# Kernel tuning notes

Measured on AMD Instinct MI355X. Metric: run time of the kernel, lower is better.

The kernel has to match this reference:

```python
import jax, jax.numpy as jnp
import numpy as np

N_NODES = 100000
C = 128
E = 800000
V = 50000
NEG_SLOPE = 0.2


def gat_conv(x, edges, W, att_src, att_dst, bias, num_nodes):
    """Single-head PyG-style GATConv with self-loops added (PyG default).

    edges: [2, E] with row 0 = source j, row 1 = destination i.
    """
    loops = jnp.arange(num_nodes, dtype=edges.dtype)
    src = jnp.concatenate([edges[0], loops])  # [E+N]
    dst = jnp.concatenate([edges[1], loops])

    h = x @ W.T                               # [N, C] linear transform
    a_s = h @ att_src                         # [N] per-node src score
    a_d = h @ att_dst                         # [N] per-node dst score

    e = jax.nn.leaky_relu(a_s[src] + a_d[dst], NEG_SLOPE)  # [E+N]
    # scatter-softmax over edges grouped by destination node
    m = jax.ops.segment_max(e, dst, num_segments=num_nodes)
    ex = jnp.exp(e - m[dst])
    denom = jax.ops.segment_sum(ex, dst, num_segments=num_nodes)
    alpha = ex / (denom[dst] + 1e-16)         # [E+N]

    out = jax.ops.segment_sum(alpha[:, None] * h[src], dst, num_segments=num_nodes)
    return out + bias


def setup_inputs() -> dict:
    key = jax.random.key(0)
    ks = jax.random.split(key, 12)
    s = 1.0 / np.sqrt(C)
    return {
        "embedding": jax.random.normal(ks[0], (N_NODES, C), jnp.float32),
        "W1": jax.random.normal(ks[1], (C, C), jnp.float32) * s,
        "att_src1": jax.random.normal(ks[2], (C,), jnp.float32) * s,
        "att_dst1": jax.random.normal(ks[3], (C,), jnp.float32) * s,
        "b1": jax.random.normal(ks[4], (C,), jnp.float32) * s,
        "W2": jax.random.normal(ks[5], (C, C), jnp.float32) * s,
        "att_src2": jax.random.normal(ks[6], (C,), jnp.float32) * s,
        "att_dst2": jax.random.normal(ks[7], (C,), jnp.float32) * s,
        "b2": jax.random.normal(ks[8], (C,), jnp.float32) * s,
        "edges1": jax.random.randint(ks[9], (2, E), 0, N_NODES, jnp.int64 if jax.config.jax_enable_x64 else jnp.int32),
        "edges2": jax.random.randint(ks[10], (2, E), 0, N_NODES, jnp.int64 if jax.config.jax_enable_x64 else jnp.int32),
        "idx_mapping": jax.random.randint(ks[11], (V,), 0, N_NODES, jnp.int64 if jax.config.jax_enable_x64 else jnp.int32),
    }


def reference(embedding, W1, att_src1, att_dst1, b1, W2, att_src2, att_dst2, b2,
              edges1, edges2, idx_mapping):
    h = gat_conv(embedding, edges1, W1, att_src1, att_dst1, b1, N_NODES)
    h = gat_conv(h, edges2, W2, att_src2, att_dst2, b2, N_NODES)
    return h[idx_mapping]
```

## Files before the change

kernel.cpp:

```cpp
#include <hip/hip_runtime.h>

#define N_NODES 100000
#define C_DIM 128
#define E_EDGES 800000
#define V_OUT 50000
#define EN (E_EDGES + N_NODES)
#define M2 (2 * N_NODES)
#define EN2 (2 * EN)

#define BSHIFT 9
#define NBUCK_L ((N_NODES + 511) >> 9)
#define NBUCK2 (2 * NBUCK_L)
#define CAP 8192
#define P1_CHUNK 4096
#define P1_PER_T (P1_CHUNK / 256)
#define NCHUNK ((EN2 + P1_CHUNK - 1) / P1_CHUNK)

typedef unsigned int uint;
typedef unsigned short ushort;
typedef __attribute__((ext_vector_type(8))) short bf16x8;
typedef __attribute__((ext_vector_type(4))) float f32x4;

static __device__ __forceinline__ ushort f2bf(float f) {
    uint u = __float_as_uint(f);
    u += 0x7fffu + ((u >> 16) & 1);
    return (ushort)(u >> 16);
}

__global__ void f2bf_kernel(const float* __restrict__ in, ushort* __restrict__ out, int n4)
{
    int i = blockIdx.x * 256 + threadIdx.x;
    if (i >= n4) return;
    float4 v = reinterpret_cast<const float4*>(in)[i];
    ushort4 r;
    r.x = f2bf(v.x); r.y = f2bf(v.y); r.z = f2bf(v.z); r.w = f2bf(v.w);
    reinterpret_cast<ushort4*>(out)[i] = r;
}

__global__ void vflag_kernel(const int* __restrict__ idx, int* __restrict__ vflag)
{
    int v = blockIdx.x * 256 + threadIdx.x;
    if (v < V_OUT) vflag[idx[v]] = 1;
}

template <int IN_F32>
__global__ __launch_bounds__(256) void gemm_mfma(
    const void* __restrict__ xin, const ushort* __restrict__ Wb,
    const float* __restrict__ att_s, const float* __restrict__ att_d,
    ushort* __restrict__ hb, float* __restrict__ a_s, float* __restrict__ a_d)
{
    const int lane = threadIdx.x & 63;
    const int wv   = threadIdx.x >> 6;
    const int nb   = (blockIdx.x * 4 + wv) * 16;
    if (nb >= N_NODES) return;
    const int m    = lane & 15;
    const int quad = lane >> 4;

    bf16x8 a[4];
    if (IN_F32) {
        const float* xrow = (const float*)xin + (long)(nb + m) * 128 + quad * 8;
        #pragma unroll
        for (int ki = 0; ki < 4; ++ki) {
            float4 u = *reinterpret_cast<const float4*>(xrow + ki * 32);
            float4 v = *reinterpret_cast<const float4*>(xrow + ki * 32 + 4);
            bf16x8 t;
            t[0] = (short)f2bf(u.x); t[1] = (short)f2bf(u.y);
            t[2] = (short)f2bf(u.z); t[3] = (short)f2bf(u.w);
            t[4] = (short)f2bf(v.x); t[5] = (short)f2bf(v.y);
            t[6] = (short)f2bf(v.z); t[7] = (short)f2bf(v.w);
            a[ki] = t;
        }
    } else {
        const ushort* xrow = (const ushort*)xin + (long)(nb + m) * 128 + quad * 8;
        #pragma unroll
        for (int ki = 0; ki < 4; ++ki)
            a[ki] = *reinterpret_cast<const bf16x8*>(xrow + ki * 32);
    }

    float ps[4] = {0, 0, 0, 0}, pd[4] = {0, 0, 0, 0};

    #pragma unroll
    for (int ct = 0; ct < 8; ++ct) {
        const int c = ct * 16 + m;
        const ushort* wrow = Wb + (long)c * 128 + quad * 8;
        f32x4 acc = {0.f, 0.f, 0.f, 0.f};
        #pragma unroll
        for (int ki = 0; ki < 4; ++ki) {
            bf16x8 b = *reinterpret_cast<const bf16x8*>(wrow + ki * 32);
            acc = __builtin_amdgcn_mfma_f32_16x16x32_bf16(a[ki], b, acc, 0, 0, 0);
        }
        const float asc = att_s[c], adc = att_d[c];
        #pragma unroll
        for (int r = 0; r < 4; ++r) {
            const int node = nb + quad * 4 + r;
            hb[(long)node * 128 + c] = f2bf(acc[r]);
            ps[r] = fmaf(acc[r], asc, ps[r]);
            pd[r] = fmaf(acc[r], adc, pd[r]);
        }
    }
    #pragma unroll
    for (int r = 0; r < 4; ++r) {
        float s = ps[r], d = pd[r];
        #pragma unroll
        for (int x = 1; x < 16; x <<= 1) { s += __shfl_xor(s, x); d += __shfl_xor(d, x); }
        if (m == 0) {
            const int node = nb + quad * 4 + r;
            a_s[node] = s; a_d[node] = d;
        }
    }
}

__global__ __launch_bounds__(256) void partition_kernel(
    const int* __restrict__ e1, const int* __restrict__ e2,
    int* __restrict__ cursor, uint* __restrict__ slab)
{
    __shared__ int cnt[NBUCK2];
    __shared__ int basearr[NBUCK2];
    const int tid = threadIdx.x;
    for (int i = tid; i < NBUCK2; i += 256) cnt[i] = 0;
    __syncthreads();

    const int e0 = blockIdx.x * P1_CHUNK;
    uint ent[P1_PER_T];
    int  bkt[P1_PER_T];
    #pragma unroll
    for (int i = 0; i < P1_PER_T; ++i) {
        int e = e0 + i * 256 + tid;
        bkt[i] = -1;
        if (e < EN2) {
            int src, dst, lb;
            if (e < EN) {
                if (e < E_EDGES) { src = e1[e]; dst = e1[E_EDGES + e]; }
                else             { src = dst = e - E_EDGES; }
                lb = 0;
            } else {
                int f = e - EN;
                if (f < E_EDGES) { src = e2[f]; dst = e2[E_EDGES + f]; }
                else             { src = dst = f - E_EDGES; }
                lb = NBUCK_L;
            }
            bkt[i] = lb + (dst >> BSHIFT);
            ent[i] = (uint)src | ((uint)(dst & 511) << 17);
            atomicAdd(&cnt[bkt[i]], 1);
        }
    }
    __syncthreads();
    for (int b = tid; b < NBUCK2; b += 256) {
        int c = cnt[b];
        basearr[b] = (c > 0) ? atomicAdd(&cursor[b], c) : 0;
        cnt[b] = 0;
    }
    __syncthreads();
    #pragma unroll
    for (int i = 0; i < P1_PER_T; ++i) {
        if (bkt[i] >= 0) {
            int r = basearr[bkt[i]] + atomicAdd(&cnt[bkt[i]], 1);
            if (r < CAP) slab[(long)bkt[i] * CAP + r] = ent[i];
        }
    }
}

__global__ void bucket_scan(const int* __restrict__ cursor, int* __restrict__ bbase)
{
    const int lane = threadIdx.x;
    int v[7]; int s = 0;
    #pragma unroll
    for (int i = 0; i < 7; ++i) {
        int idx = lane * 7 + i;
        v[i] = (idx < NBUCK2) ? cursor[idx] : 0;
        s += v[i];
    }
    int incl = s;
    #pragma unroll
    for (int d = 1; d < 64; d <<= 1) {
        int t = __shfl_up(incl, d);
        if (lane >= d) incl += t;
    }
    int excl = incl - s;
    #pragma unroll
    for (int i = 0; i < 7; ++i) {
        int idx = lane * 7 + i;
        if (idx < NBUCK2) bbase[idx] = excl;
        excl += v[i];
    }
}

__global__ __launch_bounds__(256) void local_csr(
    const uint* __restrict__ slab, const int* __restrict__ cursor,
    const int* __restrict__ bbase, int* __restrict__ offs, int* __restrict__ esrc)
{
    __shared__ uint ent[CAP];
    __shared__ int deg[512];
    __shared__ int excl[512];
    const int b = blockIdx.x;
    const int tid = threadIdx.x;
    const int cnt = min(cursor[b], CAP);
    const int base = bbase[b];
    const int layer = (b >= NBUCK_L);
    const int node0 = (b - layer * NBUCK_L) << BSHIFT;
    const int obase = layer * N_NODES;
    const int nodes_n = min(512, N_NODES - node0);

    for (int i = tid; i < 512; i += 256) deg[i] = 0;
    __syncthreads();
    for (int i = tid; i < cnt; i += 256) {
        uint v = slab[(long)b * CAP + i];
        ent[i] = v;
        atomicAdd(&deg[v >> 17], 1);
    }
    __syncthreads();
    if (tid < 64) {
        int v8[8]; int s = 0;
        #pragma unroll
        for (int i = 0; i < 8; ++i) { v8[i] = deg[tid * 8 + i]; s += v8[i]; }
        int incl = s;
        #pragma unroll
        for (int d = 1; d < 64; d <<= 1) {
            int t = __shfl_up(incl, d);
            if (tid >= d) incl += t;
        }
        int e = incl - s;
        #pragma unroll
        for (int i = 0; i < 8; ++i) { excl[tid * 8 + i] = e; e += v8[i]; }
    }
    __syncthreads();
    for (int i = tid; i < nodes_n; i += 256)
        offs[obase + node0 + i] = base + excl[i];
    for (int i = tid; i < 512; i += 256) deg[i] = 0;
    if (tid == 0 && node0 + 512 >= N_NODES)
        offs[obase + N_NODES] = base + cnt;
    __syncthreads();
    for (int i = tid; i < cnt; i += 256) {
        uint v = ent[i];
        int dl = v >> 17;
        int r = atomicAdd(&deg[dl], 1);
        esrc[base + excl[dl] + r] = (int)(v & 0x1ffff);
    }
}

template <int MODE>
__global__ __launch_bounds__(256) void aggregate(
    const ushort* __restrict__ hb, const float* __restrict__ a_s,
    const float* __restrict__ a_d, const float* __restrict__ bias,
    const int* __restrict__ offs, const int* __restrict__ esrc,
    const int* __restrict__ vflag, void* __restrict__ outp, int obase)
{
    const int wave = threadIdx.x >> 6;
    const int lane = threadIdx.x & 63;
    const int node = blockIdx.x * 4 + wave;
    if (MODE == 1 && vflag[node] == 0) return;

    const int r   = lane >> 4;
    const int c16 = lane & 15;
    const int start = offs[obase + node];
    const int end   = offs[obase + node + 1];
    const float ad  = a_d[node];

    float acc[8] = {0, 0, 0, 0, 0, 0, 0, 0};
    float dsum = 0.0f;

    for (int j0 = start; j0 < end; j0 += 64) {
        int j = j0 + lane;
        int cnt = min(64, end - j0);
        int s_l = 0;
        float w_l = 0.0f;
        if (j < end) {
            s_l = esrc[j];
            float e = a_s[s_l] + ad;
            e = (e >= 0.0f) ? e : 0.2f * e;
            w_l = __expf(e);
            dsum += w_l;
        }
        for (int jj = 0; jj < cnt; jj += 8) {
            int   i0 = jj + r,            i1 = jj + 4 + r;
            float w0 = __shfl(w_l, i0);
            int   s0 = __shfl(s_l, i0);
            float w1 = __shfl(w_l, i1);
            int   s1 = __shfl(s_l, i1);
            const uint4 h0 = *reinterpret_cast<const uint4*>(hb + ((long)s0 << 7) + (c16 << 3));
            const uint4 h1 = *reinterpret_cast<const uint4*>(hb + ((long)s1 << 7) + (c16 << 3));
            acc[0] = fmaf(w0, __uint_as_float(h0.x << 16),          acc[0]);
            acc[1] = fmaf(w0, __uint_as_float(h0.x & 0xffff0000u),  acc[1]);
            acc[2] = fmaf(w0, __uint_as_float(h0.y << 16),          acc[2]);
            acc[3] = fmaf(w0, __uint_as_float(h0.y & 0xffff0000u),  acc[3]);
            acc[4] = fmaf(w0, __uint_as_float(h0.z << 16),          acc[4]);
            acc[5] = fmaf(w0, __uint_as_float(h0.z & 0xffff0000u),  acc[5]);
            acc[6] = fmaf(w0, __uint_as_float(h0.w << 16),          acc[6]);
            acc[7] = fmaf(w0, __uint_as_float(h0.w & 0xffff0000u),  acc[7]);
            acc[0] = fmaf(w1, __uint_as_float(h1.x << 16),          acc[0]);
            acc[1] = fmaf(w1, __uint_as_float(h1.x & 0xffff0000u),  acc[1]);
            acc[2] = fmaf(w1, __uint_as_float(h1.y << 16),          acc[2]);
            acc[3] = fmaf(w1, __uint_as_float(h1.y & 0xffff0000u),  acc[3]);
            acc[4] = fmaf(w1, __uint_as_float(h1.z << 16),          acc[4]);
            acc[5] = fmaf(w1, __uint_as_float(h1.z & 0xffff0000u),  acc[5]);
            acc[6] = fmaf(w1, __uint_as_float(h1.w << 16),          acc[6]);
            acc[7] = fmaf(w1, __uint_as_float(h1.w & 0xffff0000u),  acc[7]);
        }
    }
    #pragma unroll
    for (int d = 1; d < 64; d <<= 1) dsum += __shfl_xor(dsum, d);
    const float inv = 1.0f / (dsum + 1e-16f);

    #pragma unroll
    for (int k = 0; k < 8; ++k) {
        acc[k] += __shfl_xor(acc[k], 16);
        acc[k] += __shfl_xor(acc[k], 32);
    }

    if (r == 0) {
        const int c0 = c16 << 3;
        const float4 b0 = *reinterpret_cast<const float4*>(bias + c0);
        const float4 b1 = *reinterpret_cast<const float4*>(bias + c0 + 4);
        float res[8];
        res[0] = fmaf(acc[0], inv, b0.x);
        res[1] = fmaf(acc[1], inv, b0.y);
        res[2] = fmaf(acc[2], inv, b0.z);
        res[3] = fmaf(acc[3], inv, b0.w);
        res[4] = fmaf(acc[4], inv, b1.x);
        res[5] = fmaf(acc[5], inv, b1.y);
        res[6] = fmaf(acc[6], inv, b1.z);
        res[7] = fmaf(acc[7], inv, b1.w);
        if (MODE == 0) {
            uint4 pk;
            pk.x = (uint)f2bf(res[0]) | ((uint)f2bf(res[1]) << 16);
            pk.y = (uint)f2bf(res[2]) | ((uint)f2bf(res[3]) << 16);
            pk.z = (uint)f2bf(res[4]) | ((uint)f2bf(res[5]) << 16);
            pk.w = (uint)f2bf(res[6]) | ((uint)f2bf(res[7]) << 16);
            *reinterpret_cast<uint4*>((ushort*)outp + ((long)node << 7) + c0) = pk;
        } else {
            float* op = (float*)outp + ((long)node << 7) + c0;
            *reinterpret_cast<float4*>(op)     = make_float4(res[0], res[1], res[2], res[3]);
            *reinterpret_cast<float4*>(op + 4) = make_float4(res[4], res[5], res[6], res[7]);
        }
    }
}

__global__ void gather_out(const float* __restrict__ h, const int* __restrict__ idx,
                           float* __restrict__ out)
{
    int g = blockIdx.x * 256 + threadIdx.x;
    int v = g >> 5, c4 = (g & 31) << 2;
    long src = (long)idx[v] * C_DIM + c4;
    *reinterpret_cast<float4*>(out + ((long)v * C_DIM + c4)) =
        *reinterpret_cast<const float4*>(h + src);
}

extern "C" void kernel_launch(void* const* d_in, const int* in_sizes, int n_in,
                              void* d_out, int out_size, void* d_ws, size_t ws_size,
                              hipStream_t stream)
{
    const float* emb = (const float*)d_in[0];
    const float* W1  = (const float*)d_in[1];
    const float* as1 = (const float*)d_in[2];
    const float* ad1 = (const float*)d_in[3];
    const float* b1  = (const float*)d_in[4];
    const float* W2  = (const float*)d_in[5];
    const float* as2 = (const float*)d_in[6];
    const float* ad2 = (const float*)d_in[7];
    const float* b2  = (const float*)d_in[8];
    const int* edges1 = (const int*)d_in[9];
    const int* edges2 = (const int*)d_in[10];
    const int* idxm   = (const int*)d_in[11];
    float* out = (float*)d_out;

    char* p = (char*)d_ws;
    auto alloc = [&](size_t bytes) {
        char* r = p;
        p += (bytes + 255) & ~(size_t)255;
        return r;
    };
    float*  hB   = (float*)alloc((size_t)N_NODES * C_DIM * 4);
    ushort* hb   = (ushort*)alloc((size_t)N_NODES * C_DIM * 2);
    ushort* a1o  = (ushort*)alloc((size_t)N_NODES * C_DIM * 2);
    uint*   slab = (uint*)alloc((size_t)NBUCK2 * CAP * 4);
    int*    esrc = (int*)alloc((size_t)EN2 * 4);
    int*    offs = (int*)alloc((size_t)(M2 + 1) * 4);
    ushort* W1b  = (ushort*)alloc((size_t)C_DIM * C_DIM * 2);
    ushort* W2b  = (ushort*)alloc((size_t)C_DIM * C_DIM * 2);
    float*  aS   = (float*)alloc((size_t)N_NODES * 4);
    float*  aD   = (float*)alloc((size_t)N_NODES * 4);
    int*  cursor = (int*)alloc((size_t)NBUCK2 * 4);
    int*  bbase  = (int*)alloc((size_t)NBUCK2 * 4);
    int*  vflag  = (int*)alloc((size_t)N_NODES * 4);

    f2bf_kernel<<<(C_DIM * C_DIM / 4 + 255) / 256, 256, 0, stream>>>(W1, W1b, C_DIM * C_DIM / 4);
    f2bf_kernel<<<(C_DIM * C_DIM / 4 + 255) / 256, 256, 0, stream>>>(W2, W2b, C_DIM * C_DIM / 4);
    hipMemsetAsync(vflag, 0, (size_t)N_NODES * 4, stream);
    vflag_kernel<<<(V_OUT + 255) / 256, 256, 0, stream>>>(idxm, vflag);

    hipMemsetAsync(cursor, 0, (size_t)NBUCK2 * 4, stream);
    partition_kernel<<<NCHUNK, 256, 0, stream>>>(edges1, edges2, cursor, slab);
    bucket_scan<<<1, 64, 0, stream>>>(cursor, bbase);
    local_csr<<<NBUCK2, 256, 0, stream>>>(slab, cursor, bbase, offs, esrc);

    gemm_mfma<1><<<(N_NODES / 16 + 3) / 4, 256, 0, stream>>>(emb, W1b, as1, ad1, hb, aS, aD);
    aggregate<0><<<N_NODES / 4, 256, 0, stream>>>(hb, aS, aD, b1, offs, esrc, vflag, a1o, 0);

    gemm_mfma<0><<<(N_NODES / 16 + 3) / 4, 256, 0, stream>>>(a1o, W2b, as2, ad2, hb, aS, aD);
    aggregate<1><<<N_NODES / 4, 256, 0, stream>>>(hb, aS, aD, b2, offs, esrc, vflag, hB, N_NODES);

    gather_out<<<(V_OUT * 32) / 256, 256, 0, stream>>>(hB, idxm, out);
}
```

Before: 312.4 us.

## Precompute edge weights in separate pass and aggregate one node per quarter-wave

```diff
diff --git a/kernel.cpp b/kernel.cpp
--- a/kernel.cpp
+++ b/kernel.cpp
@@ -187,7 +187,7 @@
 
 __global__ __launch_bounds__(256) void local_csr(
     const uint* __restrict__ slab, const int* __restrict__ cursor,
-    const int* __restrict__ bbase, int* __restrict__ offs, int* __restrict__ esrc)
+    const int* __restrict__ bbase, int* __restrict__ offs, uint* __restrict__ esrc)
 {
     __shared__ uint ent[CAP];
     __shared__ int deg[512];
@@ -234,104 +234,105 @@
         uint v = ent[i];
         int dl = v >> 17;
         int r = atomicAdd(&deg[dl], 1);
-        esrc[base + excl[dl] + r] = (int)(v & 0x1ffff);
+        esrc[base + excl[dl] + r] = v;
+    }
+}
+
+__global__ __launch_bounds__(256) void weights_kernel(
+    const float* __restrict__ a_s, const float* __restrict__ a_d,
+    const uint* __restrict__ esrc, const int* __restrict__ cursor,
+    const int* __restrict__ bbase, float* __restrict__ wv, int bucket0)
+{
+    const int b = bucket0 + (blockIdx.x >> 2);
+    const int cnt = min(cursor[b], CAP);
+    const int base = bbase[b];
+    const int node0 = (b - bucket0) << BSHIFT;
+    for (int i = (blockIdx.x & 3) * 256 + threadIdx.x; i < cnt; i += 1024) {
+        uint v = esrc[base + i];
+        float e = a_s[v & 0x1ffff] + a_d[node0 + (v >> 17)];
+        e = (e >= 0.0f) ? e : 0.2f * e;
+        wv[base + i] = __expf(e);
     }
 }
 
 template <int MODE>
 __global__ __launch_bounds__(256) void aggregate(
-    const ushort* __restrict__ hb, const float* __restrict__ a_s,
-    const float* __restrict__ a_d, const float* __restrict__ bias,
-    const int* __restrict__ offs, const int* __restrict__ esrc,
+    const ushort* __restrict__ hb, const float* __restrict__ wv,
+    const float* __restrict__ bias,
+    const int* __restrict__ offs, const uint* __restrict__ esrc,
     const int* __restrict__ vflag, void* __restrict__ outp, int obase)
 {
     const int wave = threadIdx.x >> 6;
     const int lane = threadIdx.x & 63;
-    const int node = blockIdx.x * 4 + wave;
-    if (MODE == 1 && vflag[node] == 0) return;
-
-    const int r   = lane >> 4;
-    const int c16 = lane & 15;
-    const int start = offs[obase + node];
-    const int end   = offs[obase + node + 1];
-    const float ad  = a_d[node];
-
+    const int slot = lane >> 4;
+    const int c16  = lane & 15;
+    const int node = (blockIdx.x * 4 + wave) * 4 + slot;
+
+    int start = offs[obase + node];
+    int end   = offs[obase + node + 1];
+    bool active = true;
+    if (MODE == 1) { active = (vflag[node] != 0); if (!active) end = start; }
+
+    const long coff = (long)(c16 << 3);
     float acc[8] = {0, 0, 0, 0, 0, 0, 0, 0};
     float dsum = 0.0f;
 
-    for (int j0 = start; j0 < end; j0 += 64) {
-        int j = j0 + lane;
-        int cnt = min(64, end - j0);
-        int s_l = 0;
-        float w_l = 0.0f;
-        if (j < end) {
-            s_l = esrc[j];
-            float e = a_s[s_l] + ad;
-            e = (e >= 0.0f) ? e : 0.2f * e;
-            w_l = __expf(e);
-            dsum += w_l;
-        }
-        for (int jj = 0; jj < cnt; jj += 8) {
-            int   i0 = jj + r,            i1 = jj + 4 + r;
-            float w0 = __shfl(w_l, i0);
-            int   s0 = __shfl(s_l, i0);
-            float w1 = __shfl(w_l, i1);
-            int   s1 = __shfl(s_l, i1);
-            const uint4 h0 = *reinterpret_cast<const uint4*>(hb + ((long)s0 << 7) + (c16 << 3));
-            const uint4 h1 = *reinterpret_cast<const uint4*>(hb + ((long)s1 << 7) + (c16 << 3));
-            acc[0] = fmaf(w0, __uint_as_float(h0.x << 16),          acc[0]);
-            acc[1] = fmaf(w0, __uint_as_float(h0.x & 0xffff0000u),  acc[1]);
-            acc[2] = fmaf(w0, __uint_as_float(h0.y << 16),          acc[2]);
-            acc[3] = fmaf(w0, __uint_as_float(h0.y & 0xffff0000u),  acc[3]);
-            acc[4] = fmaf(w0, __uint_as_float(h0.z << 16),          acc[4]);
-            acc[5] = fmaf(w0, __uint_as_float(h0.z & 0xffff0000u),  acc[5]);
-            acc[6] = fmaf(w0, __uint_as_float(h0.w << 16),          acc[6]);
-            acc[7] = fmaf(w0, __uint_as_float(h0.w & 0xffff0000u),  acc[7]);
-            acc[0] = fmaf(w1, __uint_as_float(h1.x << 16),          acc[0]);
-            acc[1] = fmaf(w1, __uint_as_float(h1.x & 0xffff0000u),  acc[1]);
-            acc[2] = fmaf(w1, __uint_as_float(h1.y << 16),          acc[2]);
-            acc[3] = fmaf(w1, __uint_as_float(h1.y & 0xffff0000u),  acc[3]);
-            acc[4] = fmaf(w1, __uint_as_float(h1.z << 16),          acc[4]);
-            acc[5] = fmaf(w1, __uint_as_float(h1.z & 0xffff0000u),  acc[5]);
-            acc[6] = fmaf(w1, __uint_as_float(h1.w << 16),          acc[6]);
-            acc[7] = fmaf(w1, __uint_as_float(h1.w & 0xffff0000u),  acc[7]);
-        }
-    }
-    #pragma unroll
-    for (int d = 1; d < 64; d <<= 1) dsum += __shfl_xor(dsum, d);
+    if (start < end) {
+        const int e1 = end - 1;
+        uint v1 = 0; float w0, w1; uint4 h0;
+        {
+            uint v0 = esrc[start];
+            w0 = wv[start];
+            int jc = min(start + 1, e1);
+            v1 = esrc[jc];
+            w1 = (start + 1 < end) ? wv[jc] : 0.0f;
+            h0 = *reinterpret_cast<const uint4*>(hb + ((long)(v0 & 0x1ffff) << 7) + coff);
+        }
+        for (int j = start; j < end; ++j) {
+            const int j2 = j + 2;
+            const int jc = min(j2, e1);
+            uint  v2 = esrc[jc];
+            float w2 = (j2 < end) ? wv[jc] : 0.0f;
+            uint4 h1 = *reinterpret_cast<const uint4*>(hb + ((long)(v1 & 0x1ffff) << 7) + coff);
+            dsum += w0;
+            acc[0] = fmaf(w0, __uint_as_float(h0.x << 16),         acc[0]);
+            acc[1] = fmaf(w0, __uint_as_float(h0.x & 0xffff0000u), acc[1]);
+            acc[2] = fmaf(w0, __uint_as_float(h0.y << 16),         acc[2]);
+            acc[3] = fmaf(w0, __uint_as_float(h0.y & 0xffff0000u), acc[3]);
+            acc[4] = fmaf(w0, __uint_as_float(h0.z << 16),         acc[4]);
+            acc[5] = fmaf(w0, __uint_as_float(h0.z & 0xffff0000u), acc[5]);
+            acc[6] = fmaf(w0, __uint_as_float(h0.w << 16),         acc[6]);
+            acc[7] = fmaf(w0, __uint_as_float(h0.w & 0xffff0000u), acc[7]);
+            w0 = w1; h0 = h1; v1 = v2; w1 = w2;
+        }
+    }
+
+    if (MODE == 1 && !active) return;
+
     const float inv = 1.0f / (dsum + 1e-16f);
-
-    #pragma unroll
-    for (int k = 0; k < 8; ++k) {
-        acc[k] += __shfl_xor(acc[k], 16);
-        acc[k] += __shfl_xor(acc[k], 32);
-    }
-
-    if (r == 0) {
-        const int c0 = c16 << 3;
-        const float4 b0 = *reinterpret_cast<const float4*>(bias + c0);
-        const float4 b1 = *reinterpret_cast<const float4*>(bias + c0 + 4);
-        float res[8];
-        res[0] = fmaf(acc[0], inv, b0.x);
-        res[1] = fmaf(acc[1], inv, b0.y);
-        res[2] = fmaf(acc[2], inv, b0.z);
-        res[3] = fmaf(acc[3], inv, b0.w);
-        res[4] = fmaf(acc[4], inv, b1.x);
-        res[5] = fmaf(acc[5], inv, b1.y);
-        res[6] = fmaf(acc[6], inv, b1.z);
-        res[7] = fmaf(acc[7], inv, b1.w);
-        if (MODE == 0) {
-            uint4 pk;
-            pk.x = (uint)f2bf(res[0]) | ((uint)f2bf(res[1]) << 16);
-            pk.y = (uint)f2bf(res[2]) | ((uint)f2bf(res[3]) << 16);
-            pk.z = (uint)f2bf(res[4]) | ((uint)f2bf(res[5]) << 16);
-            pk.w = (uint)f2bf(res[6]) | ((uint)f2bf(res[7]) << 16);
-            *reinterpret_cast<uint4*>((ushort*)outp + ((long)node << 7) + c0) = pk;
-        } else {
-            float* op = (float*)outp + ((long)node << 7) + c0;
-            *reinterpret_cast<float4*>(op)     = make_float4(res[0], res[1], res[2], res[3]);
-            *reinterpret_cast<float4*>(op + 4) = make_float4(res[4], res[5], res[6], res[7]);
-        }
+    const int c0 = c16 << 3;
+    const float4 b0 = *reinterpret_cast<const float4*>(bias + c0);
+    const float4 b1 = *reinterpret_cast<const float4*>(bias + c0 + 4);
+    float res[8];
+    res[0] = fmaf(acc[0], inv, b0.x);
+    res[1] = fmaf(acc[1], inv, b0.y);
+    res[2] = fmaf(acc[2], inv, b0.z);
+    res[3] = fmaf(acc[3], inv, b0.w);
+    res[4] = fmaf(acc[4], inv, b1.x);
+    res[5] = fmaf(acc[5], inv, b1.y);
+    res[6] = fmaf(acc[6], inv, b1.z);
+    res[7] = fmaf(acc[7], inv, b1.w);
+    if (MODE == 0) {
+        uint4 pk;
+        pk.x = (uint)f2bf(res[0]) | ((uint)f2bf(res[1]) << 16);
+        pk.y = (uint)f2bf(res[2]) | ((uint)f2bf(res[3]) << 16);
+        pk.z = (uint)f2bf(res[4]) | ((uint)f2bf(res[5]) << 16);
+        pk.w = (uint)f2bf(res[6]) | ((uint)f2bf(res[7]) << 16);
+        *reinterpret_cast<uint4*>((ushort*)outp + ((long)node << 7) + c0) = pk;
+    } else {
+        float* op = (float*)outp + ((long)node << 7) + c0;
+        *reinterpret_cast<float4*>(op)     = make_float4(res[0], res[1], res[2], res[3]);
+        *reinterpret_cast<float4*>(op + 4) = make_float4(res[4], res[5], res[6], res[7]);
     }
 }
 
@@ -373,31 +374,33 @@
     ushort* hb   = (ushort*)alloc((size_t)N_NODES * C_DIM * 2);
     ushort* a1o  = (ushort*)alloc((size_t)N_NODES * C_DIM * 2);
     uint*   slab = (uint*)alloc((size_t)NBUCK2 * CAP * 4);
-    int*    esrc = (int*)alloc((size_t)EN2 * 4);
+    uint*   esrc = (uint*)alloc((size_t)EN2 * 4);
+    float*  wvb  = (float*)alloc((size_t)EN2 * 4);
     int*    offs = (int*)alloc((size_t)(M2 + 1) * 4);
     ushort* W1b  = (ushort*)alloc((size_t)C_DIM * C_DIM * 2);
     ushort* W2b  = (ushort*)alloc((size_t)C_DIM * C_DIM * 2);
     float*  aS   = (float*)alloc((size_t)N_NODES * 4);
     float*  aD   = (float*)alloc((size_t)N_NODES * 4);
+    int*  bbase  = (int*)alloc((size_t)NBUCK2 * 4);
     int*  cursor = (int*)alloc((size_t)NBUCK2 * 4);
-    int*  bbase  = (int*)alloc((size_t)NBUCK2 * 4);
     int*  vflag  = (int*)alloc((size_t)N_NODES * 4);
 
+    hipMemsetAsync(cursor, 0, (size_t)((char*)vflag - (char*)cursor) + (size_t)N_NODES * 4, stream);
     f2bf_kernel<<<(C_DIM * C_DIM / 4 + 255) / 256, 256, 0, stream>>>(W1, W1b, C_DIM * C_DIM / 4);
     f2bf_kernel<<<(C_DIM * C_DIM / 4 + 255) / 256, 256, 0, stream>>>(W2, W2b, C_DIM * C_DIM / 4);
-    hipMemsetAsync(vflag, 0, (size_t)N_NODES * 4, stream);
     vflag_kernel<<<(V_OUT + 255) / 256, 256, 0, stream>>>(idxm, vflag);
 
-    hipMemsetAsync(cursor, 0, (size_t)NBUCK2 * 4, stream);
     partition_kernel<<<NCHUNK, 256, 0, stream>>>(edges1, edges2, cursor, slab);
     bucket_scan<<<1, 64, 0, stream>>>(cursor, bbase);
     local_csr<<<NBUCK2, 256, 0, stream>>>(slab, cursor, bbase, offs, esrc);
 
     gemm_mfma<1><<<(N_NODES / 16 + 3) / 4, 256, 0, stream>>>(emb, W1b, as1, ad1, hb, aS, aD);
-    aggregate<0><<<N_NODES / 4, 256, 0, stream>>>(hb, aS, aD, b1, offs, esrc, vflag, a1o, 0);
+    weights_kernel<<<NBUCK_L * 4, 256, 0, stream>>>(aS, aD, esrc, cursor, bbase, wvb, 0);
+    aggregate<0><<<N_NODES / 16, 256, 0, stream>>>(hb, wvb, b1, offs, esrc, vflag, a1o, 0);
 
     gemm_mfma<0><<<(N_NODES / 16 + 3) / 4, 256, 0, stream>>>(a1o, W2b, as2, ad2, hb, aS, aD);
-    aggregate<1><<<N_NODES / 4, 256, 0, stream>>>(hb, aS, aD, b2, offs, esrc, vflag, hB, N_NODES);
+    weights_kernel<<<NBUCK_L * 4, 256, 0, stream>>>(aS, aD, esrc, cursor, bbase, wvb, NBUCK_L);
+    aggregate<1><<<N_NODES / 16, 256, 0, stream>>>(hb, wvb, b2, offs, esrc, vflag, hB, N_NODES);
 
     gather_out<<<(V_OUT * 32) / 256, 256, 0, stream>>>(hB, idxm, out);
 }
```

Result: slower. 319.1 us (+2.2%).
